# Performance work log

Hardware: AMD Instinct MI355X
Metric: run time of the kernel (lower is better)

Reference implementation:

```python
import jax, jax.numpy as jnp
import numpy as np

N_REGIONS = 20000
N_EMB = 5
N_INT = 5

def setup_inputs() -> dict:
    key = jax.random.key(0)
    k1, k2, k3, k4, k5, k6 = jax.random.split(key, 6)
    cell_region_embedding = jax.random.normal(k1, (4096, 4096, N_EMB), dtype=jnp.float32)
    region_ix = jax.random.randint(k2, (4096,), 0, N_REGIONS, dtype=jnp.int64)
    # per-region parameter tables (original inits to 0; randn for meaningful test)
    weight1 = jax.random.normal(k3, (N_REGIONS, N_EMB, N_INT), dtype=jnp.float32) * 0.1
    bias1 = jax.random.normal(k4, (N_REGIONS, N_INT), dtype=jnp.float32) * 0.1
    weight2 = jax.random.normal(k5, (N_REGIONS, N_INT, 1), dtype=jnp.float32) * 0.1
    bias2 = jax.random.normal(k6, (N_REGIONS, 1), dtype=jnp.float32) * 0.1
    return {
        "cell_region_embedding": cell_region_embedding,
        "region_ix": region_ix,
        "weight1": weight1,
        "bias1": bias1,
        "weight2": weight2,
        "bias2": bias2,
    }

def reference(cell_region_embedding, region_ix, weight1, bias1, weight2, bias2):
    # gather per-region params: [b, c, d] and [b, d]
    w1 = weight1[region_ix]   # [regions_b, n_emb, n_int]
    b1 = bias1[region_ix]     # [regions_b, n_int]
    w2 = weight2[region_ix]   # [regions_b, n_int, 1]
    b2 = bias2[region_ix]     # [regions_b, 1]
    # linear1 + sigmoid: [cells, regions_b, n_int]
    h = jax.nn.sigmoid(jnp.einsum('abc,bcd->abd', cell_region_embedding, w1) + b1)
    # linear2, squeeze last dim: [cells, regions_b]
    out = (jnp.einsum('abc,bcd->abd', h, w2) + b2).squeeze(-1)
    return out
```

## Files before the change

kernel.cpp:

```cpp
#include <hip/hip_runtime.h>
#include <hip/hip_bf16.h>


#define NA 4096
#define NB 4096
#define NE 5
#define NI 5
#define ROWS 32

__global__ __launch_bounds__(256) void e2e_kernel(
    const float* __restrict__ E,
    const int*   __restrict__ rix,
    const float* __restrict__ w1,
    const float* __restrict__ b1,
    const float* __restrict__ w2,
    const float* __restrict__ b2,
    float*       __restrict__ out)
{
    const int b  = blockIdx.x * 256 + threadIdx.x;
    const int a0 = blockIdx.y * ROWS;

    const int r = rix[b];

    float W1[NE][NI];
    const float* w1p = w1 + (size_t)r * (NE * NI);
#pragma unroll
    for (int c = 0; c < NE; ++c)
#pragma unroll
        for (int d = 0; d < NI; ++d)
            W1[c][d] = w1p[c * NI + d];

    float B1[NI], W2[NI];
    const float* b1p = b1 + (size_t)r * NI;
    const float* w2p = w2 + (size_t)r * NI;
#pragma unroll
    for (int d = 0; d < NI; ++d) {
        B1[d] = b1p[d];
        W2[d] = w2p[d];
    }
    const float B2 = b2[r];

    const float* erow = E + ((size_t)a0 * NB + (size_t)b) * NE;
    float*       orow = out + (size_t)a0 * NB + b;

#pragma unroll 4
    for (int i = 0; i < ROWS; ++i) {
        const float e0 = erow[0];
        const float e1 = erow[1];
        const float e2 = erow[2];
        const float e3 = erow[3];
        const float e4 = erow[4];

        float acc = B2;
#pragma unroll
        for (int d = 0; d < NI; ++d) {
            float h = B1[d]
                    + e0 * W1[0][d]
                    + e1 * W1[1][d]
                    + e2 * W1[2][d]
                    + e3 * W1[3][d]
                    + e4 * W1[4][d];
            h = 1.0f / (1.0f + __expf(-h));
            acc += h * W2[d];
        }
        *orow = acc;

        erow += (size_t)NB * NE;
        orow += NB;
    }
}

extern "C" void kernel_launch(void* const* d_in, const int* in_sizes, int n_in,
                              void* d_out, int out_size, void* d_ws, size_t ws_size,
                              hipStream_t stream) {
    const float* E   = (const float*)d_in[0];
    const int*   rix = (const int*)  d_in[1];
    const float* w1  = (const float*)d_in[2];
    const float* b1  = (const float*)d_in[3];
    const float* w2  = (const float*)d_in[4];
    const float* b2  = (const float*)d_in[5];
    float*       out = (float*)d_out;

    dim3 grid(NB / 256, NA / ROWS);
    dim3 block(256);
    hipLaunchKernelGGL(e2e_kernel, grid, block, 0, stream, E, rix, w1, b1, w2, b2, out);
}
```

Before: 478.7 us.

## Stage embedding rows through LDS with coalesced float4 loads

Each wavefront now loads one full 256-column embedding row segment into shared memory using coalesced float4 loads. Threads then read their five values from LDS, replacing strided 5-float global loads per thread. This improves global coalescing but adds two barriers per chunk, gives up overlap between loads and compute, and brings LDS bank conflicts from the stride-5 reads.

```diff
diff --git a/kernel.cpp b/kernel.cpp
--- a/kernel.cpp
+++ b/kernel.cpp
@@ -7,6 +7,8 @@
 #define NE 5
 #define NI 5
 #define ROWS 32
+#define SROWS 4
+#define ROW_FLOATS (256 * NE)
 
 __global__ __launch_bounds__(256) void e2e_kernel(
     const float* __restrict__ E,
@@ -17,8 +19,14 @@
     const float* __restrict__ b2,
     float*       __restrict__ out)
 {
-    const int b  = blockIdx.x * 256 + threadIdx.x;
-    const int a0 = blockIdx.y * ROWS;
+    __shared__ float lds[SROWS * ROW_FLOATS];
+
+    const int tid  = threadIdx.x;
+    const int b0   = blockIdx.x * 256;
+    const int b    = b0 + tid;
+    const int a0   = blockIdx.y * ROWS;
+    const int srow = tid >> 6;
+    const int lane = tid & 63;
 
     const int r = rix[b];
 
@@ -40,33 +48,38 @@
     }
     const float B2 = b2[r];
 
-    const float* erow = E + ((size_t)a0 * NB + (size_t)b) * NE;
-    float*       orow = out + (size_t)a0 * NB + b;
+#pragma unroll 1
+    for (int chunk = 0; chunk < ROWS / SROWS; ++chunk) {
+        const int a_ld = a0 + chunk * SROWS + srow;
+        const float4* src = (const float4*)(E + ((size_t)a_ld * NB + b0) * NE);
+        float4* dst = (float4*)(lds + srow * ROW_FLOATS);
+#pragma unroll
+        for (int j = 0; j < ROW_FLOATS / 4 / 64; ++j)
+            dst[lane + j * 64] = src[lane + j * 64];
 
-#pragma unroll 4
-    for (int i = 0; i < ROWS; ++i) {
-        const float e0 = erow[0];
-        const float e1 = erow[1];
-        const float e2 = erow[2];
-        const float e3 = erow[3];
-        const float e4 = erow[4];
+        __syncthreads();
 
-        float acc = B2;
 #pragma unroll
-        for (int d = 0; d < NI; ++d) {
-            float h = B1[d]
-                    + e0 * W1[0][d]
-                    + e1 * W1[1][d]
-                    + e2 * W1[2][d]
-                    + e3 * W1[3][d]
-                    + e4 * W1[4][d];
-            h = 1.0f / (1.0f + __expf(-h));
-            acc += h * W2[d];
+        for (int s = 0; s < SROWS; ++s) {
+            const float* e = lds + s * ROW_FLOATS + tid * NE;
+            const float e0 = e[0], e1 = e[1], e2 = e[2], e3 = e[3], e4 = e[4];
+
+            float acc = B2;
+#pragma unroll
+            for (int d = 0; d < NI; ++d) {
+                float h = B1[d]
+                        + e0 * W1[0][d]
+                        + e1 * W1[1][d]
+                        + e2 * W1[2][d]
+                        + e3 * W1[3][d]
+                        + e4 * W1[4][d];
+                h = 1.0f / (1.0f + __expf(-h));
+                acc += h * W2[d];
+            }
+            out[(size_t)(a0 + chunk * SROWS + s) * NB + b] = acc;
         }
-        *orow = acc;
 
-        erow += (size_t)NB * NE;
-        orow += NB;
+        __syncthreads();
     }
 }
 
```

After: 476.1 us. About the same (-0.5%).
